# Kernel tuning notes

Measured on AMD Instinct MI355X. Metric: run time of the kernel, lower is better.

Reference implementation:

```python
import jax, jax.numpy as jnp
import numpy as np
import math

D_MODEL = 768
N_HEADS = 6
HD = D_MODEL // N_HEADS  # 128
RANK = D_MODEL // 4      # 192
B, T = 128, 256


def _rope_tables(T, dim):
    # matches torch: inv = 1/10000**(arange(0,dim,2)/dim); emb = cat([outer(t,inv)]*2, -1)
    inv = 1.0 / (10000.0 ** (jnp.arange(0, dim, 2, dtype=jnp.float32) / dim))
    t = jnp.arange(T, dtype=jnp.float32)
    freqs = jnp.outer(t, inv)                       # [T, dim/2]
    emb = jnp.concatenate([freqs, freqs], axis=-1)  # [T, dim]
    return jnp.cos(emb), jnp.sin(emb)               # each [T, dim]


def _rot(x):
    h = x.shape[-1] // 2
    return jnp.concatenate([-x[..., h:], x[..., :h]], axis=-1)


def setup_inputs() -> dict:
    key = jax.random.key(0)
    ks = jax.random.split(key, 8)
    s_in = 1.0 / math.sqrt(D_MODEL)
    s_r = 1.0 / math.sqrt(RANK)
    inp = {
        'x': jax.random.normal(ks[0], (B, T, D_MODEL), dtype=jnp.float32),
        'qA': jax.random.normal(ks[1], (D_MODEL, RANK), dtype=jnp.float32) * s_in,
        'qB': jax.random.normal(ks[2], (RANK, D_MODEL), dtype=jnp.float32) * s_r,
        'kA': jax.random.normal(ks[3], (D_MODEL, RANK), dtype=jnp.float32) * s_in,
        'kB': jax.random.normal(ks[4], (RANK, D_MODEL), dtype=jnp.float32) * s_r,
        'vA': jax.random.normal(ks[5], (D_MODEL, RANK), dtype=jnp.float32) * s_in,
        'vB': jax.random.normal(ks[6], (RANK, D_MODEL), dtype=jnp.float32) * s_r,
        'o_w': jax.random.normal(ks[7], (D_MODEL, D_MODEL), dtype=jnp.float32) * s_in,
    }
    return inp


def reference(x, qA, qB, kA, kB, vA, vB, o_w):
    Bb, Tt, _ = x.shape
    # low-rank projections: in -> rank -> out, then split heads [B, H, T, hd]
    def proj(A, W):
        h = (x @ A) @ W
        return h.reshape(Bb, Tt, N_HEADS, HD).transpose(0, 2, 1, 3)
    q = proj(qA, qB)
    k = proj(kA, kB)
    v = proj(vA, vB)
    cos, sin = _rope_tables(Tt, HD)  # [T, hd], broadcast over B, H
    q = q * cos + _rot(q) * sin
    k = k * cos + _rot(k) * sin
    att = jnp.einsum('bhqd,bhkd->bhqk', q, k) / math.sqrt(HD)
    causal = jnp.tril(jnp.ones((Tt, Tt), dtype=bool))
    att = jnp.where(causal, att, -jnp.inf)
    att = jax.nn.softmax(att, axis=-1)
    out = jnp.einsum('bhqk,bhkd->bhqd', att, v)          # [B, H, T, hd]
    out = out.transpose(0, 2, 1, 3).reshape(Bb, Tt, D_MODEL)
    return out @ o_w
```

## Files before the change

### kernel.cpp

```cpp
#include <hip/hip_runtime.h>
#include <hip/hip_bf16.h>
#include <stdint.h>

typedef __attribute__((ext_vector_type(8))) short s16x8;
typedef __attribute__((ext_vector_type(4))) float f32x4;

#define D_MODEL 768
#define N_HEADS 6
#define HD 128
#define RANK 192
#define TT 256
#define NROW 32768
#define QKV_LD 2304
#define NK 12
#define QSCL 0.08838834764831845f

__device__ inline short f2bf(float f) {
  union { float f; unsigned u; } x; x.f = f;
  unsigned r = x.u + 0x7fffu + ((x.u >> 16) & 1u);
  return (short)(r >> 16);
}
__device__ inline float bf2f(short v) {
  union { unsigned u; float f; } x; x.u = ((unsigned)(unsigned short)v) << 16;
  return x.f;
}
__device__ inline void gload_lds16(const void* g, void* lds) {
  __builtin_amdgcn_global_load_lds(
      (const __attribute__((address_space(1))) unsigned int*)g,
      (__attribute__((address_space(3))) unsigned int*)lds, 16, 0, 0);
}

#define BAR()    asm volatile("s_barrier" ::: "memory")
#define LGKM0()  asm volatile("s_waitcnt lgkmcnt(0)" ::: "memory")
#define WAITVM4() asm volatile("s_waitcnt vmcnt(4)" ::: "memory")
#define WAITVM0() asm volatile("s_waitcnt vmcnt(0)" ::: "memory")

__global__ void k_tables(float* __restrict__ cosT, float* __restrict__ sinT) {
  int tid = blockIdx.x * 256 + threadIdx.x;
  int t = tid >> 6, i = tid & 63;
  float inv = powf(10000.0f, -(float)i / 64.0f);
  float ang = (float)t * inv;
  cosT[tid] = cosf(ang);
  sinT[tid] = sinf(ang);
}

__global__ void k_castx(const float* __restrict__ x, short* __restrict__ xb) {
  int t = blockIdx.x * 256 + threadIdx.x;
  const float4* xp = (const float4*)x;
  float4 a = xp[t * 2], b = xp[t * 2 + 1];
  s16x8 o;
  o[0] = f2bf(a.x); o[1] = f2bf(a.y); o[2] = f2bf(a.z); o[3] = f2bf(a.w);
  o[4] = f2bf(b.x); o[5] = f2bf(b.y); o[6] = f2bf(b.z); o[7] = f2bf(b.w);
  *(s16x8*)(xb + (size_t)t * 8) = o;
}

__global__ void k_makew(const float* __restrict__ qA, const float* __restrict__ qB,
                        const float* __restrict__ kA, const float* __restrict__ kB,
                        const float* __restrict__ vA, const float* __restrict__ vB,
                        short* __restrict__ WT) {
  int g = blockIdx.x * 256 + threadIdx.x;
  int n4 = g % 576, kkb = g / 576;
  int part = n4 / 192, nnb = (n4 % 192) * 4;
  const float* A = (part == 0) ? qA : (part == 1) ? kA : vA;
  const float* Bm = (part == 0) ? qB : (part == 1) ? kB : vB;
  float acc[4][4] = {};
  for (int r0 = 0; r0 < RANK; r0 += 4) {
    float4 a4[4], b4[4];
#pragma unroll
    for (int q = 0; q < 4; ++q)
      a4[q] = *(const float4*)&A[(kkb + q * 192) * RANK + r0];
#pragma unroll
    for (int i = 0; i < 4; ++i)
      b4[i] = *(const float4*)&Bm[(r0 + i) * 768 + nnb];
#pragma unroll
    for (int q = 0; q < 4; ++q) {
      const float* aq = (const float*)&a4[q];
#pragma unroll
      for (int i = 0; i < 4; ++i) {
        const float* bi = (const float*)&b4[i];
#pragma unroll
        for (int jn = 0; jn < 4; ++jn)
          acc[q][jn] += aq[i] * bi[jn];
      }
    }
  }
#pragma unroll
  for (int q = 0; q < 4; ++q)
#pragma unroll
    for (int jn = 0; jn < 4; ++jn)
      WT[(size_t)(part * 768 + nnb + jn) * 768 + kkb + q * 192] = f2bf(acc[q][jn]);
}

__global__ void k_wot(const float* __restrict__ ow, short* __restrict__ WT) {
  int g = blockIdx.x * 256 + threadIdx.x;
  int n = g % 768, kk = g / 768;
  WT[(size_t)(2304 + n) * 768 + kk] = f2bf(ow[(size_t)kk * 768 + n]);
}

__device__ inline s16x8 rdfrag(const short* hbase, int rowbyte, int ksl4x, int swz) {
  return *(const s16x8*)((const char*)hbase + rowbyte + (((ksl4x) ^ (swz)) << 4));
}

template <bool OUTBF>
__global__ __launch_bounds__(512, 2) void k_gemm8(const short* __restrict__ A,
                                                  const short* __restrict__ Bt,
                                                  void* __restrict__ Cv, int ldc) {
  extern __shared__ short lds[];
  const int tid = threadIdx.x;
  const int wid = tid >> 6, lane = tid & 63;
  const int l15 = lane & 15, l4 = lane >> 4;
  const int wr = wid >> 2, wc = wid & 3;
  const int swz = l15 & 7;
  const int bid = blockIdx.y * 128 + blockIdx.x;
  const int cpx = (gridDim.y * 128) >> 3;
  const int sbid = (bid & 7) * cpx + (bid >> 3);
  const long mbase = (long)(sbid & 127) * 256;
  const long nbase = (long)(sbid >> 7) * 256;

  const int hb0 = wid * 2048 + lane * 16;
  const int hb1 = hb0 + 1024;
  const int r0 = hb0 >> 7, c0 = ((hb0 >> 4) & 7) ^ (r0 & 7);
  const int r1 = hb1 >> 7, c1 = ((hb1 >> 4) & 7) ^ (r1 & 7);
  const int off0 = r0 * 768 + c0 * 8;
  const int off1 = r1 * 768 + c1 * 8;

#define STAGE(G, rowoff, kt, ldsS) do {                                        \
    gload_lds16((G) + (size_t)(rowoff) * 768 + (kt) * 64 + off0,               \
                (char*)(ldsS) + wid * 2048);                                   \
    gload_lds16((G) + (size_t)(rowoff) * 768 + (kt) * 64 + off1,               \
                (char*)(ldsS) + wid * 2048 + 1024);                            \
  } while (0)

#define LDSA(buf, half) (lds + ((buf) * 2 + (half)) * 8192)
#define LDSB(buf, half) (lds + 32768 + ((buf) * 2 + (half)) * 8192)

  f32x4 acc[8][4] = {};

  STAGE(A,  mbase,       0, LDSA(0, 0));
  STAGE(Bt, nbase,       0, LDSB(0, 0));
  STAGE(A,  mbase + 128, 0, LDSA(0, 1));
  STAGE(Bt, nbase + 128, 0, LDSB(0, 1));
  STAGE(A,  mbase,       1, LDSA(1, 0));
  STAGE(Bt, nbase,       1, LDSB(1, 0));
  WAITVM4();
  BAR();

  s16x8 a03[4][2], a47[4][2], b01[2][2], b23[2][2];

#pragma unroll
  for (int kt = 0; kt < NK; ++kt) {
    const int buf = kt & 1, nbuf = buf ^ 1;
    const short* Ab = LDSA(buf, wr);
    const short* Bb = LDSB(buf, (wc >> 1));
    const int browbase = (wc & 1) * 64 * 128;

#pragma unroll
    for (int mf = 0; mf < 4; ++mf)
#pragma unroll
      for (int ks = 0; ks < 2; ++ks)
        a03[mf][ks] = rdfrag(Ab, (mf * 16 + l15) * 128, ks * 4 + l4, swz);
#pragma unroll
    for (int nf = 0; nf < 2; ++nf)
#pragma unroll
      for (int ks = 0; ks < 2; ++ks)
        b01[nf][ks] = rdfrag(Bb, browbase + (nf * 16 + l15) * 128, ks * 4 + l4, swz);
    if (kt + 1 < NK) STAGE(A, mbase + 128, kt + 1, LDSA(nbuf, 1));
    BAR();
    LGKM0();
    __builtin_amdgcn_s_setprio(1);
#pragma unroll
    for (int mf = 0; mf < 4; ++mf)
#pragma unroll
      for (int nf = 0; nf < 2; ++nf)
#pragma unroll
        for (int ks = 0; ks < 2; ++ks)
          acc[mf][nf] = __builtin_amdgcn_mfma_f32_16x16x32_bf16(a03[mf][ks], b01[nf][ks], acc[mf][nf], 0, 0, 0);
    __builtin_amdgcn_s_setprio(0);
    BAR();

#pragma unroll
    for (int mf = 0; mf < 4; ++mf)
#pragma unroll
      for (int ks = 0; ks < 2; ++ks)
        a47[mf][ks] = rdfrag(Ab, ((mf + 4) * 16 + l15) * 128, ks * 4 + l4, swz);
    if (kt + 1 < NK) STAGE(Bt, nbase + 128, kt + 1, LDSB(nbuf, 1));
    BAR();
    LGKM0();
    __builtin_amdgcn_s_setprio(1);
#pragma unroll
    for (int mf = 0; mf < 4; ++mf)
#pragma unroll
      for (int nf = 0; nf < 2; ++nf)
#pragma unroll
        for (int ks = 0; ks < 2; ++ks)
          acc[mf + 4][nf] = __builtin_amdgcn_mfma_f32_16x16x32_bf16(a47[mf][ks], b01[nf][ks], acc[mf + 4][nf], 0, 0, 0);
    __builtin_amdgcn_s_setprio(0);
    BAR();

#pragma unroll
    for (int nf = 0; nf < 2; ++nf)
#pragma unroll
      for (int ks = 0; ks < 2; ++ks)
        b23[nf][ks] = rdfrag(Bb, browbase + ((nf + 2) * 16 + l15) * 128, ks * 4 + l4, swz);
    if (kt + 2 < NK) STAGE(A, mbase, kt + 2, LDSA(buf, 0));
    BAR();
    LGKM0();
    __builtin_amdgcn_s_setprio(1);
#pragma unroll
    for (int mf = 0; mf < 4; ++mf)
#pragma unroll
      for (int nf = 0; nf < 2; ++nf)
#pragma unroll
        for (int ks = 0; ks < 2; ++ks)
          acc[mf][nf + 2] = __builtin_amdgcn_mfma_f32_16x16x32_bf16(a03[mf][ks], b23[nf][ks], acc[mf][nf + 2], 0, 0, 0);
    __builtin_amdgcn_s_setprio(0);
    BAR();

    if (kt + 2 < NK) STAGE(Bt, nbase, kt + 2, LDSB(buf, 0));
    BAR();
    __builtin_amdgcn_s_setprio(1);
#pragma unroll
    for (int mf = 0; mf < 4; ++mf)
#pragma unroll
      for (int nf = 0; nf < 2; ++nf)
#pragma unroll
        for (int ks = 0; ks < 2; ++ks)
          acc[mf + 4][nf + 2] = __builtin_amdgcn_mfma_f32_16x16x32_bf16(a47[mf][ks], b23[nf][ks], acc[mf + 4][nf + 2], 0, 0, 0);
    __builtin_amdgcn_s_setprio(0);
    if (kt < NK - 1) {
      if (kt + 2 < NK) WAITVM4(); else WAITVM0();
      BAR();
    }
  }
#undef STAGE

#pragma unroll
  for (int mf = 0; mf < 8; ++mf)
#pragma unroll
    for (int nf = 0; nf < 4; ++nf)
#pragma unroll
      for (int r = 0; r < 4; ++r) {
        long row = mbase + wr * 128 + mf * 16 + l4 * 4 + r;
        long col = nbase + wc * 64 + nf * 16 + l15;
        if (OUTBF) ((short*)Cv)[row * ldc + col] = f2bf(acc[mf][nf][r]);
        else       ((float*)Cv)[row * ldc + col] = acc[mf][nf][r];
      }
}

__global__ void k_ropek(short* __restrict__ qkv, const float* __restrict__ cosT,
                        const float* __restrict__ sinT) {
  int tid = blockIdx.x * 256 + threadIdx.x;
  int row = tid / 48, rem = tid % 48;
  int head = rem >> 3, i8 = (rem & 7) * 8;
  int t = row & (TT - 1);
  size_t base = (size_t)row * QKV_LD + D_MODEL + head * 128 + i8;
  s16x8 a = *(const s16x8*)(qkv + base);
  s16x8 b = *(const s16x8*)(qkv + base + 64);
  const float4* cp = (const float4*)(cosT + t * 64 + i8);
  const float4* sp = (const float4*)(sinT + t * 64 + i8);
  float4 c04 = cp[0], c14 = cp[1], s04 = sp[0], s14 = sp[1];
  float cs[8] = {c04.x, c04.y, c04.z, c04.w, c14.x, c14.y, c14.z, c14.w};
  float sn[8] = {s04.x, s04.y, s04.z, s04.w, s14.x, s14.y, s14.z, s14.w};
  s16x8 na, nb;
#pragma unroll
  for (int j = 0; j < 8; ++j) {
    float av = bf2f(a[j]), bv = bf2f(b[j]);
    na[j] = f2bf(av * cs[j] - bv * sn[j]);
    nb[j] = f2bf(bv * cs[j] + av * sn[j]);
  }
  *(s16x8*)(qkv + base) = na;
  *(s16x8*)(qkv + base + 64) = nb;
}

__global__ __launch_bounds__(512) void k_attn(const short* __restrict__ qkv,
                                              short* __restrict__ attout,
                                              const float* __restrict__ cosT,
                                              const float* __restrict__ sinT) {
  __shared__ short Kls[64 * 128];
  __shared__ short Vt[128 * 64];
  __shared__ short Pls[8][32 * 64];
  const int tid = threadIdx.x;
  const int wid = tid >> 6, lane = tid & 63;
  const int l15 = lane & 15, l4 = lane >> 4;
  const int b = blockIdx.x / N_HEADS, h = blockIdx.x % N_HEADS;
  const long row0 = (long)b * TT;

  s16x8 qf[2][4];
#pragma unroll
  for (int mi = 0; mi < 2; ++mi)
#pragma unroll
    for (int kc = 0; kc < 4; ++kc) {
      long row = row0 + wid * 32 + mi * 16 + l15;
      qf[mi][kc] = *(const s16x8*)(qkv + row * QKV_LD + h * HD + kc * 32 + l4 * 8);
    }
#pragma unroll
  for (int mi = 0; mi < 2; ++mi) {
    int t = wid * 32 + mi * 16 + l15;
#pragma unroll
    for (int kc = 0; kc < 2; ++kc) {
      const float4* cp = (const float4*)(cosT + t * 64 + kc * 32 + l4 * 8);
      const float4* sp = (const float4*)(sinT + t * 64 + kc * 32 + l4 * 8);
      float4 c04 = cp[0], c14 = cp[1], s04 = sp[0], s14 = sp[1];
      float cs[8] = {c04.x, c04.y, c04.z, c04.w, c14.x, c14.y, c14.z, c14.w};
      float sn[8] = {s04.x, s04.y, s04.z, s04.w, s14.x, s14.y, s14.z, s14.w};
#pragma unroll
      for (int jj = 0; jj < 8; ++jj) {
        float av = bf2f(qf[mi][kc][jj]);
        float bv = bf2f(qf[mi][kc + 2][jj]);
        qf[mi][kc][jj]     = f2bf((av * cs[jj] - bv * sn[jj]) * QSCL);
        qf[mi][kc + 2][jj] = f2bf((bv * cs[jj] + av * sn[jj]) * QSCL);
      }
    }
  }

  float mst[2][4], lst[2][4];
  f32x4 oacc[2][8];
#pragma unroll
  for (int mi = 0; mi < 2; ++mi)
#pragma unroll
    for (int r = 0; r < 4; ++r) { mst[mi][r] = -1e30f; lst[mi][r] = 0.f; }
#pragma unroll
  for (int mi = 0; mi < 2; ++mi)
#pragma unroll
    for (int nd = 0; nd < 8; ++nd) oacc[mi][nd] = {0.f, 0.f, 0.f, 0.f};

  const int jmax = (wid * 32 + 31) / 64;
  const int d0 = wid * 16;
  for (int j = 0; j < 4; ++j) {
#pragma unroll
    for (int q2 = 0; q2 < 2; ++q2) {
      int bb = wid * 2048 + q2 * 1024 + lane * 16;
      int r = bb >> 8;
      int cpos = (bb >> 4) & 15;
      int sc = cpos ^ (r & 7);
      gload_lds16(qkv + (row0 + j * 64 + r) * QKV_LD + D_MODEL + h * HD + sc * 8,
                  (char*)Kls + wid * 2048 + q2 * 1024);
    }
    const short* vsrc = qkv + (row0 + j * 64 + lane) * QKV_LD + 2 * D_MODEL + h * HD + d0;
    s16x8 v0 = *(const s16x8*)vsrc;
    s16x8 v1 = *(const s16x8*)(vsrc + 8);
    __syncthreads();
#pragma unroll
    for (int e = 0; e < 8; ++e)
      *(short*)((char*)Vt + (d0 + e) * 128 + (((lane >> 3) ^ e) << 4) + (lane & 7) * 2) = v0[e];
#pragma unroll
    for (int e = 0; e < 8; ++e)
      *(short*)((char*)Vt + (d0 + 8 + e) * 128 + (((lane >> 3) ^ e) << 4) + (lane & 7) * 2) = v1[e];

    if (j <= jmax) {
      f32x4 sacc[2][4] = {};
#pragma unroll
      for (int kc = 0; kc < 4; ++kc) {
        s16x8 kf[4];
#pragma unroll
        for (int ni = 0; ni < 4; ++ni)
          kf[ni] = *(const s16x8*)((const char*)Kls + (ni * 16 + l15) * 256 +
                                   (((kc * 4 + l4) ^ (l15 & 7)) << 4));
#pragma unroll
        for (int mi = 0; mi < 2; ++mi)
#pragma unroll
          for (int ni = 0; ni < 4; ++ni)
            sacc[mi][ni] = __builtin_amdgcn_mfma_f32_16x16x32_bf16(qf[mi][kc], kf[ni], sacc[mi][ni], 0, 0, 0);
      }
#pragma unroll
      for (int mi = 0; mi < 2; ++mi) {
#pragma unroll
        for (int r = 0; r < 4; ++r) {
          int qr = wid * 32 + mi * 16 + l4 * 4 + r;
          float rm = -1e30f;
#pragma unroll
          for (int ni = 0; ni < 4; ++ni) {
            int kvc = j * 64 + ni * 16 + l15;
            if (kvc > qr) sacc[mi][ni][r] = -1e30f;
            rm = fmaxf(rm, sacc[mi][ni][r]);
          }
#pragma unroll
          for (int d2 = 1; d2 < 16; d2 <<= 1)
            rm = fmaxf(rm, __shfl_xor(rm, d2, 64));
          float mold = mst[mi][r];
          float mnew = fmaxf(mold, rm);
          float alpha = __expf(mold - mnew);
          mst[mi][r] = mnew;
          float rs = 0.f;
#pragma unroll
          for (int ni = 0; ni < 4; ++ni) {
            float p = __expf(sacc[mi][ni][r] - mnew);
            sacc[mi][ni][r] = p;
            rs += p;
          }
#pragma unroll
          for (int d2 = 1; d2 < 16; d2 <<= 1)
            rs += __shfl_xor(rs, d2, 64);
          lst[mi][r] = lst[mi][r] * alpha + rs;
#pragma unroll
          for (int nd = 0; nd < 8; ++nd)
            oacc[mi][nd][r] *= alpha;
        }
      }
#pragma unroll
      for (int mi = 0; mi < 2; ++mi)
#pragma unroll
        for (int ni = 0; ni < 4; ++ni)
#pragma unroll
          for (int r = 0; r < 4; ++r) {
            int prow = mi * 16 + l4 * 4 + r;
            int pcp = (ni * 2 + (l15 >> 3)) ^ (prow & 7);
            *(short*)((char*)Pls[wid] + prow * 128 + (pcp << 4) + (l15 & 7) * 2) =
                f2bf(sacc[mi][ni][r]);
          }
    }
    LGKM0();
    BAR();
    if (j <= jmax) {
#pragma unroll
      for (int kc2 = 0; kc2 < 2; ++kc2) {
        s16x8 pa[2];
#pragma unroll
        for (int mi = 0; mi < 2; ++mi)
          pa[mi] = *(const s16x8*)((const char*)Pls[wid] + (mi * 16 + l15) * 128 +
                                   (((kc2 * 4 + l4) ^ (l15 & 7)) << 4));
#pragma unroll
        for (int nd = 0; nd < 8; ++nd) {
          s16x8 vf = *(const s16x8*)((const char*)Vt + (nd * 16 + l15) * 128 +
                                     (((kc2 * 4 + l4) ^ (l15 & 7)) << 4));
#pragma unroll
          for (int mi = 0; mi < 2; ++mi)
            oacc[mi][nd] = __builtin_amdgcn_mfma_f32_16x16x32_bf16(pa[mi], vf, oacc[mi][nd], 0, 0, 0);
        }
      }
    }
    __syncthreads();
  }
#pragma unroll
  for (int mi = 0; mi < 2; ++mi)
#pragma unroll
    for (int nd = 0; nd < 8; ++nd)
#pragma unroll
      for (int r = 0; r < 4; ++r) {
        long row = row0 + wid * 32 + mi * 16 + l4 * 4 + r;
        int col = h * HD + nd * 16 + l15;
        attout[row * D_MODEL + col] = f2bf(oacc[mi][nd][r] / lst[mi][r]);
      }
}

extern "C" void kernel_launch(void* const* d_in, const int* in_sizes, int n_in,
                              void* d_out, int out_size, void* d_ws, size_t ws_size,
                              hipStream_t stream) {
  const float* x  = (const float*)d_in[0];
  const float* qA = (const float*)d_in[1];
  const float* qB = (const float*)d_in[2];
  const float* kA = (const float*)d_in[3];
  const float* kB = (const float*)d_in[4];
  const float* vA = (const float*)d_in[5];
  const float* vB = (const float*)d_in[6];
  const float* ow = (const float*)d_in[7];

  char* ws = (char*)d_ws;
  short* qkv   = (short*)ws;
  short* xb    = (short*)(ws + 150994944);
  short* WT    = (short*)(ws + 201326592);
  float* cosT  = (float*)(ws + 206045184);
  float* sinT  = (float*)(ws + 206110720);
  short* attout = xb;

  hipFuncSetAttribute((const void*)k_gemm8<true>,
                      hipFuncAttributeMaxDynamicSharedMemorySize, 131072);
  hipFuncSetAttribute((const void*)k_gemm8<false>,
                      hipFuncAttributeMaxDynamicSharedMemorySize, 131072);

  k_tables<<<64, 256, 0, stream>>>(cosT, sinT);
  k_castx<<<12288, 256, 0, stream>>>(x, xb);
  k_makew<<<432, 256, 0, stream>>>(qA, qB, kA, kB, vA, vB, WT);
  k_wot<<<2304, 256, 0, stream>>>(ow, WT);
  k_gemm8<true><<<dim3(128, 9), 512, 131072, stream>>>(xb, WT, (void*)qkv, QKV_LD);
  k_ropek<<<6144, 256, 0, stream>>>(qkv, cosT, sinT);
  k_attn<<<768, 512, 0, stream>>>(qkv, attout, cosT, sinT);
  k_gemm8<false><<<dim3(128, 3), 512, 131072, stream>>>(attout, WT + (size_t)2304 * 768, d_out, 768);
}
```

Before: 383.8 us.

## Double-buffer K/V loads in attention and remap GEMM tile order per XCD

The attention kernel now double-buffers K tiles in LDS and prefetches V rows into registers for the next key block, which removes one of the two barriers per iteration and overlaps global loads with compute. Shared memory becomes dynamic (80KB), which may limit blocks per CU. Separately, the GEMM block-to-tile mapping is changed so that each XCD handles a contiguous range of M tiles and iterates over all N tiles, aiming for better L2 reuse of A rows.

```diff
diff --git a/kernel.cpp b/kernel.cpp
--- a/kernel.cpp
+++ b/kernel.cpp
@@ -112,10 +112,13 @@
   const int wr = wid >> 2, wc = wid & 3;
   const int swz = l15 & 7;
   const int bid = blockIdx.y * 128 + blockIdx.x;
-  const int cpx = (gridDim.y * 128) >> 3;
-  const int sbid = (bid & 7) * cpx + (bid >> 3);
-  const long mbase = (long)(sbid & 127) * 256;
-  const long nbase = (long)(sbid >> 7) * 256;
+  const int nper = gridDim.y;
+  const int xcd = bid & 7, loc = bid >> 3;
+  const int mq = loc / nper;
+  const int mt = xcd * 16 + mq;
+  const int nt = loc - mq * nper;
+  const long mbase = (long)mt * 256;
+  const long nbase = (long)nt * 256;
 
   const int hb0 = wid * 2048 + lane * 16;
   const int hb1 = hb0 + 1024;
@@ -276,14 +279,18 @@
                                               short* __restrict__ attout,
                                               const float* __restrict__ cosT,
                                               const float* __restrict__ sinT) {
-  __shared__ short Kls[64 * 128];
-  __shared__ short Vt[128 * 64];
-  __shared__ short Pls[8][32 * 64];
+  extern __shared__ short smem[];
+  short* Kls0 = smem;
+  short* Kls1 = smem + 8192;
+  short* Vt   = smem + 16384;
+  short* PlsW;
   const int tid = threadIdx.x;
   const int wid = tid >> 6, lane = tid & 63;
   const int l15 = lane & 15, l4 = lane >> 4;
+  PlsW = smem + 24576 + wid * 2048;
   const int b = blockIdx.x / N_HEADS, h = blockIdx.x % N_HEADS;
   const long row0 = (long)b * TT;
+  const int d0 = wid * 16;
 
   s16x8 qf[2][4];
 #pragma unroll
@@ -313,6 +320,23 @@
     }
   }
 
+#define STAGEK(j_, Kd) do {                                                     \
+    int bb0_ = wid * 2048 + lane * 16;                                          \
+    int r0_ = bb0_ >> 8; int sc0_ = ((bb0_ >> 4) & 15) ^ (r0_ & 7);             \
+    gload_lds16(qkv + (row0 + (j_) * 64 + r0_) * QKV_LD + D_MODEL + h * HD + sc0_ * 8, \
+                (char*)(Kd) + wid * 2048);                                      \
+    int bb1_ = bb0_ + 1024;                                                     \
+    int r1_ = bb1_ >> 8; int sc1_ = ((bb1_ >> 4) & 15) ^ (r1_ & 7);             \
+    gload_lds16(qkv + (row0 + (j_) * 64 + r1_) * QKV_LD + D_MODEL + h * HD + sc1_ * 8, \
+                (char*)(Kd) + wid * 2048 + 1024);                               \
+  } while (0)
+
+#define LOADV(j_, va, vb) do {                                                  \
+    const short* vsrc_ = qkv + (row0 + (j_) * 64 + lane) * QKV_LD + 2 * D_MODEL + h * HD + d0; \
+    va = *(const s16x8*)vsrc_;                                                  \
+    vb = *(const s16x8*)(vsrc_ + 8);                                            \
+  } while (0)
+
   float mst[2][4], lst[2][4];
   f32x4 oacc[2][8];
 #pragma unroll
@@ -325,27 +349,29 @@
     for (int nd = 0; nd < 8; ++nd) oacc[mi][nd] = {0.f, 0.f, 0.f, 0.f};
 
   const int jmax = (wid * 32 + 31) / 64;
-  const int d0 = wid * 16;
+
+  STAGEK(0, Kls0);
+  s16x8 vr[2][2];
+  LOADV(0, vr[0][0], vr[0][1]);
+
+#pragma unroll
   for (int j = 0; j < 4; ++j) {
-#pragma unroll
-    for (int q2 = 0; q2 < 2; ++q2) {
-      int bb = wid * 2048 + q2 * 1024 + lane * 16;
-      int r = bb >> 8;
-      int cpos = (bb >> 4) & 15;
-      int sc = cpos ^ (r & 7);
-      gload_lds16(qkv + (row0 + j * 64 + r) * QKV_LD + D_MODEL + h * HD + sc * 8,
-                  (char*)Kls + wid * 2048 + q2 * 1024);
-    }
-    const short* vsrc = qkv + (row0 + j * 64 + lane) * QKV_LD + 2 * D_MODEL + h * HD + d0;
-    s16x8 v0 = *(const s16x8*)vsrc;
-    s16x8 v1 = *(const s16x8*)(vsrc + 8);
-    __syncthreads();
+    const int buf = j & 1;
+    const short* Kb = buf ? Kls1 : Kls0;
+    short* Kn = buf ? Kls0 : Kls1;
+    if (j < 3) {
+      STAGEK(j + 1, Kn);
+      LOADV(j + 1, vr[buf ^ 1][0], vr[buf ^ 1][1]);
+    }
+    if (j < 3) WAITVM4(); else WAITVM0();
+    __builtin_amdgcn_sched_barrier(0);
+    BAR();
 #pragma unroll
     for (int e = 0; e < 8; ++e)
-      *(short*)((char*)Vt + (d0 + e) * 128 + (((lane >> 3) ^ e) << 4) + (lane & 7) * 2) = v0[e];
+      *(short*)((char*)Vt + (d0 + e) * 128 + (((lane >> 3) ^ e) << 4) + (lane & 7) * 2) = vr[buf][0][e];
 #pragma unroll
     for (int e = 0; e < 8; ++e)
-      *(short*)((char*)Vt + (d0 + 8 + e) * 128 + (((lane >> 3) ^ e) << 4) + (lane & 7) * 2) = v1[e];
+      *(short*)((char*)Vt + (d0 + 8 + e) * 128 + (((lane >> 3) ^ e) << 4) + (lane & 7) * 2) = vr[buf][1][e];
 
     if (j <= jmax) {
       f32x4 sacc[2][4] = {};
@@ -354,7 +380,7 @@
         s16x8 kf[4];
 #pragma unroll
         for (int ni = 0; ni < 4; ++ni)
-          kf[ni] = *(const s16x8*)((const char*)Kls + (ni * 16 + l15) * 256 +
+          kf[ni] = *(const s16x8*)((const char*)Kb + (ni * 16 + l15) * 256 +
                                    (((kc * 4 + l4) ^ (l15 & 7)) << 4));
 #pragma unroll
         for (int mi = 0; mi < 2; ++mi)
@@ -405,19 +431,20 @@
           for (int r = 0; r < 4; ++r) {
             int prow = mi * 16 + l4 * 4 + r;
             int pcp = (ni * 2 + (l15 >> 3)) ^ (prow & 7);
-            *(short*)((char*)Pls[wid] + prow * 128 + (pcp << 4) + (l15 & 7) * 2) =
+            *(short*)((char*)PlsW + prow * 128 + (pcp << 4) + (l15 & 7) * 2) =
                 f2bf(sacc[mi][ni][r]);
           }
     }
     LGKM0();
     BAR();
+    __builtin_amdgcn_sched_barrier(0);
     if (j <= jmax) {
 #pragma unroll
       for (int kc2 = 0; kc2 < 2; ++kc2) {
         s16x8 pa[2];
 #pragma unroll
         for (int mi = 0; mi < 2; ++mi)
-          pa[mi] = *(const s16x8*)((const char*)Pls[wid] + (mi * 16 + l15) * 128 +
+          pa[mi] = *(const s16x8*)((const char*)PlsW + (mi * 16 + l15) * 128 +
                                    (((kc2 * 4 + l4) ^ (l15 & 7)) << 4));
 #pragma unroll
         for (int nd = 0; nd < 8; ++nd) {
@@ -429,8 +456,9 @@
         }
       }
     }
-    __syncthreads();
   }
+#undef STAGEK
+#undef LOADV
 #pragma unroll
   for (int mi = 0; mi < 2; ++mi)
 #pragma unroll
@@ -467,6 +495,8 @@
                       hipFuncAttributeMaxDynamicSharedMemorySize, 131072);
   hipFuncSetAttribute((const void*)k_gemm8<false>,
                       hipFuncAttributeMaxDynamicSharedMemorySize, 131072);
+  hipFuncSetAttribute((const void*)k_attn,
+                      hipFuncAttributeMaxDynamicSharedMemorySize, 81920);
 
   k_tables<<<64, 256, 0, stream>>>(cosT, sinT);
   k_castx<<<12288, 256, 0, stream>>>(x, xb);
@@ -474,6 +504,6 @@
   k_wot<<<2304, 256, 0, stream>>>(ow, WT);
   k_gemm8<true><<<dim3(128, 9), 512, 131072, stream>>>(xb, WT, (void*)qkv, QKV_LD);
   k_ropek<<<6144, 256, 0, stream>>>(qkv, cosT, sinT);
-  k_attn<<<768, 512, 0, stream>>>(qkv, attout, cosT, sinT);
+  k_attn<<<768, 512, 81920, stream>>>(qkv, attout, cosT, sinT);
   k_gemm8<false><<<dim3(128, 3), 512, 131072, stream>>>(attout, WT + (size_t)2304 * 768, d_out, 768);
 }
```

Measured after the change: 357.7 us. -6.8%, faster.
